# Kernel optimization log

Measured on AMD Instinct MI355X. Metric: run time of the kernel, lower is better.

The kernel has to match this reference:

```python
import jax, jax.numpy as jnp
import numpy as np

N_PTS = 1_000_000
RES = 512
RANK = 48
OUT = 32
INIT_SCALE = 0.1


def _plane_sample(plane, gx, gy):
    """Bilinear grid_sample, align_corners=True, border padding.
    plane: [R, Res, Res] (R=rank); gx, gy: [N] in [-1,1] -> [R, N]."""
    res = plane.shape[-1]
    px = jnp.clip((gx + 1.0) * 0.5 * (res - 1), 0.0, res - 1.0)
    py = jnp.clip((gy + 1.0) * 0.5 * (res - 1), 0.0, res - 1.0)
    x0 = jnp.floor(px).astype(jnp.int32)
    y0 = jnp.floor(py).astype(jnp.int32)
    x1 = jnp.minimum(x0 + 1, res - 1)
    y1 = jnp.minimum(y0 + 1, res - 1)
    wx = px - x0.astype(px.dtype)
    wy = py - y0.astype(py.dtype)
    # gathers: [R, N] each
    v00 = plane[:, y0, x0]
    v01 = plane[:, y0, x1]
    v10 = plane[:, y1, x0]
    v11 = plane[:, y1, x1]
    return (v00 * (1 - wy) * (1 - wx) + v01 * (1 - wy) * wx
            + v10 * wy * (1 - wx) + v11 * wy * wx)


def _line_sample(line, gy):
    """Line is [R, Res] (width dim of size 1 collapses; x coord is 0 -> px=0).
    1-D linear interp along Res with gy in [-1,1] -> [R, N]."""
    res = line.shape[-1]
    py = jnp.clip((gy + 1.0) * 0.5 * (res - 1), 0.0, res - 1.0)
    y0 = jnp.floor(py).astype(jnp.int32)
    y1 = jnp.minimum(y0 + 1, res - 1)
    wy = py - y0.astype(py.dtype)
    return line[:, y0] * (1 - wy) + line[:, y1] * wy


def _geo_forward(coordinates, plane_xy, plane_xz, plane_yz,
                 line_z, line_y, line_x, proj_w, proj_b):
    coords = coordinates * 2.0 - 1.0  # [N, 3] in [-1, 1]
    cx, cy, cz = coords[:, 0], coords[:, 1], coords[:, 2]
    vm = (_plane_sample(plane_xy, cx, cy) * _line_sample(line_z, cz)
          + _plane_sample(plane_xz, cx, cz) * _line_sample(line_y, cy)
          + _plane_sample(plane_yz, cy, cz) * _line_sample(line_x, cx))  # [R, N]
    # projection: [N, R] @ [R, OUT] + b
    return vm.T @ proj_w.T + proj_b


def setup_inputs() -> dict:
    key = jax.random.key(0)
    ks = jax.random.split(key, 9)
    return {
        "coordinates": jax.random.uniform(ks[0], (N_PTS, 3), dtype=jnp.float32),
        "plane_xy": jax.random.normal(ks[1], (RANK, RES, RES), jnp.float32) * INIT_SCALE,
        "plane_xz": jax.random.normal(ks[2], (RANK, RES, RES), jnp.float32) * INIT_SCALE,
        "plane_yz": jax.random.normal(ks[3], (RANK, RES, RES), jnp.float32) * INIT_SCALE,
        "line_z": jax.random.normal(ks[4], (RANK, RES), jnp.float32) * INIT_SCALE,
        "line_y": jax.random.normal(ks[5], (RANK, RES), jnp.float32) * INIT_SCALE,
        "line_x": jax.random.normal(ks[6], (RANK, RES), jnp.float32) * INIT_SCALE,
        "proj_w": jax.random.normal(ks[7], (OUT, RANK), jnp.float32) * INIT_SCALE,
        "proj_b": jnp.zeros((OUT,), jnp.float32),
    }


def reference(coordinates, plane_xy, plane_xz, plane_yz,
              line_z, line_y, line_x, proj_w, proj_b):
    return _geo_forward(coordinates, plane_xy, plane_xz, plane_yz,
                        line_z, line_y, line_x, proj_w, proj_b)
```

## Files before the change

### kernel.cpp

```cpp
#include <hip/hip_runtime.h>
#include <stdint.h>

#define RES      512
#define TEXELS   (RES * RES)
#define NPTS     1000000
#define RANK     48
#define ODIM     32
#define PPB      64
#define VMS      52
#define OSTR     33
#define TT       128
#define TS       25
#define NCELL    4096
#define NB       32
#define SEG      31250
#define ENTR     (NCELL * NB)

typedef unsigned int u32;
typedef float vf4 __attribute__((ext_vector_type(4)));

__device__ __forceinline__ float lobf(u32 u) { return __uint_as_float(u << 16); }
__device__ __forceinline__ float hibf(u32 u) { return __uint_as_float(u & 0xffff0000u); }

__device__ __forceinline__ float ntl(const float* p) {
    return __builtin_nontemporal_load(p);
}
__device__ __forceinline__ vf4 ntl4(const float* p) {
    return __builtin_nontemporal_load((const vf4*)p);
}

__device__ __forceinline__ u32 pkbf(float a, float b) {
    u32 x = __float_as_uint(a), y = __float_as_uint(b);
    u32 xr = (x + 0x7fffu + ((x >> 16) & 1u)) >> 16;
    u32 yr = (y + 0x7fffu + ((y >> 16) & 1u)) & 0xffff0000u;
    return xr | yr;
}

__device__ __forceinline__ u32 sprd4(u32 a) {
    a &= 15u;
    a = (a | (a << 4)) & 0x0C3u;
    a = (a | (a << 2)) & 0x249u;
    return a;
}
__device__ __forceinline__ u32 cellOf(float x, float y, float z) {
    u32 cx = (u32)fminf(fmaxf(x * 16.f, 0.f), 15.f);
    u32 cy = (u32)fminf(fmaxf(y * 16.f, 0.f), 15.f);
    u32 cz = (u32)fminf(fmaxf(z * 16.f, 0.f), 15.f);
    return sprd4(cx) | (sprd4(cy) << 1) | (sprd4(cz) << 2);
}

template <int TEXB>
__global__ __launch_bounds__(256) void transpose_planes(
    const float* __restrict__ p0, const float* __restrict__ p1,
    const float* __restrict__ p2, char* __restrict__ ws)
{
    __shared__ u32 lds[TT * TS + 8];
    int t = threadIdx.x;
    int base = blockIdx.x * TT;
    int plane = blockIdx.y;
    const float* src = (plane == 0) ? p0 : ((plane == 1) ? p1 : p2);
    int xi = t & 31, dg = t >> 5;
#pragma unroll
    for (int j = 0; j < 3; ++j) {
        int d = dg + 8 * j;
        vf4 a = ntl4(src + (size_t)(2 * d) * TEXELS + base + 4 * xi);
        vf4 b = ntl4(src + (size_t)(2 * d + 1) * TEXELS + base + 4 * xi);
        lds[(4 * xi + 0) * TS + d] = pkbf(a.x, b.x);
        lds[(4 * xi + 1) * TS + d] = pkbf(a.y, b.y);
        lds[(4 * xi + 2) * TS + d] = pkbf(a.z, b.z);
        lds[(4 * xi + 3) * TS + d] = pkbf(a.w, b.w);
    }
    __syncthreads();
    char* outp = ws + (size_t)plane * TEXELS * TEXB + (size_t)base * TEXB;
    constexpr int NS = TT * TEXB / (16 * 256);
#pragma unroll
    for (int s = 0; s < NS; ++s) {
        u32 o = (u32)(s * 256 + t) * 16u;
        u32 texel, rem;
        if (TEXB == 128) { texel = o >> 7; rem = o & 127u; }
        else { texel = ((o >> 5) * 43691u) >> 17; rem = o - texel * 96u; }
        u32 dw = texel * TS + (rem >> 2);
        uint4 q = make_uint4(lds[dw], lds[dw + 1], lds[dw + 2], lds[dw + 3]);
        *(uint4*)(outp + o) = q;
    }
}

template <int TEXB>
__global__ __launch_bounds__(256) void transpose_lines(
    const float* __restrict__ lz, const float* __restrict__ ly,
    const float* __restrict__ lx, char* __restrict__ ws)
{
    int id = blockIdx.x * 256 + threadIdx.x;
    int line = id >> 9;
    int pos = id & (RES - 1);
    const float* src = (line == 0) ? lz : ((line == 1) ? ly : lx);
    char* dst = ws + (size_t)3 * TEXELS * TEXB + (size_t)line * RES * TEXB
                   + (size_t)pos * TEXB;
#pragma unroll
    for (int k = 0; k < 6; ++k) {
        uint4 q;
        q.x = pkbf(ntl(&src[(8 * k + 0) * RES + pos]), ntl(&src[(8 * k + 1) * RES + pos]));
        q.y = pkbf(ntl(&src[(8 * k + 2) * RES + pos]), ntl(&src[(8 * k + 3) * RES + pos]));
        q.z = pkbf(ntl(&src[(8 * k + 4) * RES + pos]), ntl(&src[(8 * k + 5) * RES + pos]));
        q.w = pkbf(ntl(&src[(8 * k + 6) * RES + pos]), ntl(&src[(8 * k + 7) * RES + pos]));
        *(uint4*)(dst + 16 * k) = q;
    }
}

__global__ __launch_bounds__(1024) void bin_count(
    const float* __restrict__ coords, u32* __restrict__ T)
{
    __shared__ u32 hist[NCELL];
    int blk = blockIdx.x, t = threadIdx.x;
#pragma unroll
    for (int i = 0; i < NCELL / 1024; ++i) hist[t + 1024 * i] = 0u;
    __syncthreads();
    int lim = (blk + 1) * SEG;
#pragma unroll 1
    for (int it = 0; it < (SEG + 1023) / 1024; ++it) {
        int idx = blk * SEG + it * 1024 + t;
        if (idx < lim) {
            float x = ntl(&coords[3 * idx + 0]);
            float y = ntl(&coords[3 * idx + 1]);
            float z = ntl(&coords[3 * idx + 2]);
            atomicAdd(&hist[cellOf(x, y, z)], 1u);
        }
    }
    __syncthreads();
#pragma unroll
    for (int i = 0; i < NCELL / 1024; ++i) {
        int cell = t + 1024 * i;
        T[(u32)cell * NB + blk] = hist[cell];
    }
}

__global__ __launch_bounds__(1024) void bin_scan(
    const u32* __restrict__ T, u32* __restrict__ C)
{
    __shared__ u32 wt[16];
    int t = threadIdx.x;
    const int PER = ENTR / 1024;
    const u32* tp = T + t * PER;
    u32 tot = 0;
#pragma unroll 16
    for (int i = 0; i < PER; ++i) tot += tp[i];
    int lane = t & 63, w = t >> 6;
    u32 incl = tot;
#pragma unroll
    for (int d = 1; d < 64; d <<= 1) {
        u32 v = __shfl_up(incl, d);
        if (lane >= d) incl += v;
    }
    if (lane == 63) wt[w] = incl;
    __syncthreads();
    u32 run = incl - tot;
#pragma unroll
    for (int i = 0; i < 16; ++i) run += (i < w) ? wt[i] : 0u;
    u32* op = C + t * PER;
#pragma unroll 16
    for (int i = 0; i < PER; ++i) { u32 v = tp[i]; op[i] = run; run += v; }
}

__global__ __launch_bounds__(1024) void bin_scatter(
    const float* __restrict__ coords, const u32* __restrict__ C,
    vf4* __restrict__ rc2)
{
    __shared__ u32 cur[NCELL];
    int blk = blockIdx.x, t = threadIdx.x;
#pragma unroll
    for (int i = 0; i < NCELL / 1024; ++i) {
        int cell = t + 1024 * i;
        cur[cell] = C[(u32)cell * NB + blk];
    }
    __syncthreads();
    int lim = (blk + 1) * SEG;
#pragma unroll 1
    for (int it = 0; it < (SEG + 1023) / 1024; ++it) {
        int idx = blk * SEG + it * 1024 + t;
        if (idx < lim) {
            float x = ntl(&coords[3 * idx + 0]);
            float y = ntl(&coords[3 * idx + 1]);
            float z = ntl(&coords[3 * idx + 2]);
            u32 pos = atomicAdd(&cur[cellOf(x, y, z)], 1u);
            vf4 v; v.x = x; v.y = y; v.z = z; v.w = __uint_as_float((u32)idx);
            __builtin_nontemporal_store(v, rc2 + pos);
        }
    }
}

__device__ __forceinline__ void prep1(float g, int& i0, int& i1, float& w) {
    float p = fminf(fmaxf((g + 1.f) * 0.5f * 511.f, 0.f), 511.f);
    float fp = floorf(p);
    i0 = (int)fp;
    i1 = min(i0 + 1, RES - 1);
    w = p - fp;
}

template <int TEXB, bool SORTED>
__global__ __launch_bounds__(512, 4) void geo_main(
    const void* __restrict__ cin, const char* __restrict__ ws,
    const float* __restrict__ W, const float* __restrict__ Bb,
    float* __restrict__ out)
{
    __shared__ float vm_lds[PPB * VMS];
    __shared__ u32 opt_lds[PPB];

    int tid = threadIdx.x;
    int ptL = tid >> 3;
    int c = tid & 7;

    int bid = blockIdx.x;
    if (SORTED) {
        int nwg = gridDim.x;
        int q = nwg >> 3, r = nwg & 7;
        int xcd = bid & 7, slot = bid >> 3;
        bid = (xcd < r ? xcd * (q + 1) : r * (q + 1) + (xcd - r) * q) + slot;
    }
    int pt = bid * PPB + ptL;

    float gx, gy, gz;
    if (SORTED) {
        vf4 cc = __builtin_nontemporal_load((const vf4*)cin + pt);
        gx = cc.x * 2.f - 1.f;
        gy = cc.y * 2.f - 1.f;
        gz = cc.z * 2.f - 1.f;
        if (c == 0) opt_lds[ptL] = __float_as_uint(cc.w);
    } else {
        const float* coords = (const float*)cin;
        gx = ntl(&coords[3 * pt + 0]) * 2.f - 1.f;
        gy = ntl(&coords[3 * pt + 1]) * 2.f - 1.f;
        gz = ntl(&coords[3 * pt + 2]) * 2.f - 1.f;
        if (c == 0) opt_lds[ptL] = (u32)pt;
    }

    int x0, x1, y0, y1, z0, z1;
    float wx, wy, wz;
    prep1(gx, x0, x1, wx);
    prep1(gy, y0, y1, wy);
    prep1(gz, z0, z1, wz);

    const size_t PW = (size_t)TEXELS * TEXB;
    const size_t LW = (size_t)RES * TEXB;
    const char* pxy = ws;
    const char* pxz = ws + PW;
    const char* pyz = ws + 2 * PW;
    const char* lzb = ws + 3 * PW;
    const char* lyb = lzb + LW;
    const char* lxb = lyb + LW;

    u32 co = 12u * (u32)c;

    u32 q[12][3], le[3][3], lf[3][3];
    {
        u32 offs[12];
        offs[0] = (u32)(y0 * RES + x0) * TEXB + co;
        offs[1] = (u32)(y0 * RES + x1) * TEXB + co;
        offs[2] = (u32)(y1 * RES + x0) * TEXB + co;
        offs[3] = (u32)(y1 * RES + x1) * TEXB + co;
        offs[4] = (u32)(z0 * RES + x0) * TEXB + co;
        offs[5] = (u32)(z0 * RES + x1) * TEXB + co;
        offs[6] = (u32)(z1 * RES + x0) * TEXB + co;
        offs[7] = (u32)(z1 * RES + x1) * TEXB + co;
        offs[8]  = (u32)(z0 * RES + y0) * TEXB + co;
        offs[9]  = (u32)(z0 * RES + y1) * TEXB + co;
        offs[10] = (u32)(z1 * RES + y0) * TEXB + co;
        offs[11] = (u32)(z1 * RES + y1) * TEXB + co;
        const char* bases[3] = { pxy, pxz, pyz };
#pragma unroll
        for (int p = 0; p < 3; ++p) {
#pragma unroll
            for (int k = 0; k < 4; ++k) {
                const u32* s = (const u32*)(bases[p] + offs[4 * p + k]);
                q[4 * p + k][0] = s[0];
                q[4 * p + k][1] = s[1];
                q[4 * p + k][2] = s[2];
            }
        }
        const char* lb[3] = { lzb, lyb, lxb };
        u32 l0[3] = { (u32)z0 * TEXB + co, (u32)y0 * TEXB + co, (u32)x0 * TEXB + co };
        u32 l1[3] = { (u32)z1 * TEXB + co, (u32)y1 * TEXB + co, (u32)x1 * TEXB + co };
#pragma unroll
        for (int p = 0; p < 3; ++p) {
            const u32* s0 = (const u32*)(lb[p] + l0[p]);
            const u32* s1 = (const u32*)(lb[p] + l1[p]);
            le[p][0] = s0[0]; le[p][1] = s0[1]; le[p][2] = s0[2];
            lf[p][0] = s1[0]; lf[p][1] = s1[1]; lf[p][2] = s1[2];
        }
    }

    float pw[3][4];
    pw[0][0] = (1.f - wy) * (1.f - wx); pw[0][1] = (1.f - wy) * wx;
    pw[0][2] = wy * (1.f - wx);         pw[0][3] = wy * wx;
    pw[1][0] = (1.f - wz) * (1.f - wx); pw[1][1] = (1.f - wz) * wx;
    pw[1][2] = wz * (1.f - wx);         pw[1][3] = wz * wx;
    pw[2][0] = (1.f - wz) * (1.f - wy); pw[2][1] = (1.f - wz) * wy;
    pw[2][2] = wz * (1.f - wy);         pw[2][3] = wz * wy;
    float lw[3] = { wz, wy, wx };

    float vm[6] = { 0.f, 0.f, 0.f, 0.f, 0.f, 0.f };
#pragma unroll
    for (int p = 0; p < 3; ++p) {
        float s0 = pw[p][0], s1 = pw[p][1], s2 = pw[p][2], s3 = pw[p][3];
        float il = 1.f - lw[p], wl = lw[p];
#pragma unroll
        for (int d = 0; d < 3; ++d) {
            u32 a = q[4 * p + 0][d], b = q[4 * p + 1][d];
            u32 cc = q[4 * p + 2][d], dd = q[4 * p + 3][d];
            float slo = s0 * lobf(a) + s1 * lobf(b) + s2 * lobf(cc) + s3 * lobf(dd);
            float shi = s0 * hibf(a) + s1 * hibf(b) + s2 * hibf(cc) + s3 * hibf(dd);
            float llo = il * lobf(le[p][d]) + wl * lobf(lf[p][d]);
            float lhi = il * hibf(le[p][d]) + wl * hibf(lf[p][d]);
            vm[2 * d + 0] = fmaf(slo, llo, vm[2 * d + 0]);
            vm[2 * d + 1] = fmaf(shi, lhi, vm[2 * d + 1]);
        }
    }

    float* vr = vm_lds + ptL * VMS + 6 * c;
    *(float2*)(vr + 0) = make_float2(vm[0], vm[1]);
    *(float2*)(vr + 2) = make_float2(vm[2], vm[3]);
    *(float2*)(vr + 4) = make_float2(vm[4], vm[5]);

    __syncthreads();

    int wav = __builtin_amdgcn_readfirstlane(tid >> 6);
    int lane = tid & 63;
    int ob = wav * 4;

    const float* vmrow = vm_lds + lane * VMS;
    float4 bb = *(const float4*)(Bb + ob);
    float a0 = bb.x, a1 = bb.y, a2 = bb.z, a3 = bb.w;
#pragma unroll 4
    for (int k = 0; k < 12; ++k) {
        float4 v = *(const float4*)(vmrow + 4 * k);
        float4 w0 = *(const float4*)(W + (ob + 0) * RANK + 4 * k);
        float4 w1 = *(const float4*)(W + (ob + 1) * RANK + 4 * k);
        float4 w2 = *(const float4*)(W + (ob + 2) * RANK + 4 * k);
        float4 w3 = *(const float4*)(W + (ob + 3) * RANK + 4 * k);
        a0 = fmaf(v.x, w0.x, a0); a0 = fmaf(v.y, w0.y, a0);
        a0 = fmaf(v.z, w0.z, a0); a0 = fmaf(v.w, w0.w, a0);
        a1 = fmaf(v.x, w1.x, a1); a1 = fmaf(v.y, w1.y, a1);
        a1 = fmaf(v.z, w1.z, a1); a1 = fmaf(v.w, w1.w, a1);
        a2 = fmaf(v.x, w2.x, a2); a2 = fmaf(v.y, w2.y, a2);
        a2 = fmaf(v.z, w2.z, a2); a2 = fmaf(v.w, w2.w, a2);
        a3 = fmaf(v.x, w3.x, a3); a3 = fmaf(v.y, w3.y, a3);
        a3 = fmaf(v.z, w3.z, a3); a3 = fmaf(v.w, w3.w, a3);
    }

    __syncthreads();
    {
        vf4 r; r.x = a0; r.y = a1; r.z = a2; r.w = a3;
        *(vf4*)(vm_lds + lane * OSTR + ob) = r;
    }
    __syncthreads();
    {
        int p8 = lane >> 3;
        int c2 = lane & 7;
        int gp = wav * 8 + p8;
        vf4 v = *(const vf4*)(vm_lds + gp * OSTR + 4 * c2);
        size_t orow = (size_t)opt_lds[gp];
        __builtin_nontemporal_store(v, (vf4*)(out + orow * ODIM + 4 * c2));
    }
}

template <int TEXB>
static void launch_unsorted(const float* coords, const float* pxy, const float* pxz,
                            const float* pyz, const float* lz, const float* ly,
                            const float* lx, const float* W, const float* Bb,
                            float* out, char* ws, hipStream_t stream) {
    dim3 gt(TEXELS / TT, 3);
    transpose_planes<TEXB><<<gt, 256, 0, stream>>>(pxy, pxz, pyz, ws);
    transpose_lines<TEXB><<<6, 256, 0, stream>>>(lz, ly, lx, ws);
    geo_main<TEXB, false><<<NPTS / PPB, 512, 0, stream>>>(coords, ws, W, Bb, out);
}

extern "C" void kernel_launch(void* const* d_in, const int* in_sizes, int n_in,
                              void* d_out, int out_size, void* d_ws, size_t ws_size,
                              hipStream_t stream) {
    const float* coords = (const float*)d_in[0];
    const float* pxy = (const float*)d_in[1];
    const float* pxz = (const float*)d_in[2];
    const float* pyz = (const float*)d_in[3];
    const float* lz = (const float*)d_in[4];
    const float* ly = (const float*)d_in[5];
    const float* lx = (const float*)d_in[6];
    const float* W = (const float*)d_in[7];
    const float* Bb = (const float*)d_in[8];
    float* out = (float*)d_out;
    char* ws = (char*)d_ws;

    size_t pool96 = (size_t)3 * TEXELS * 96 + (size_t)3 * RES * 96;
    size_t o_T = (pool96 + 255) & ~(size_t)255;
    size_t o_C = o_T + (size_t)ENTR * 4;
    size_t o_rc2 = o_C + (size_t)ENTR * 4;
    size_t need_sorted = o_rc2 + (size_t)NPTS * 16;
    size_t need128 = (size_t)3 * TEXELS * 128 + (size_t)3 * RES * 128;

    if (ws_size >= need_sorted) {
        u32* T = (u32*)(ws + o_T);
        u32* C = (u32*)(ws + o_C);
        vf4* rc2 = (vf4*)(ws + o_rc2);

        dim3 gt(TEXELS / TT, 3);
        transpose_planes<96><<<gt, 256, 0, stream>>>(pxy, pxz, pyz, ws);
        transpose_lines<96><<<6, 256, 0, stream>>>(lz, ly, lx, ws);
        bin_count<<<NB, 1024, 0, stream>>>(coords, T);
        bin_scan<<<1, 1024, 0, stream>>>(T, C);
        bin_scatter<<<NB, 1024, 0, stream>>>(coords, C, rc2);
        geo_main<96, true><<<NPTS / PPB, 512, 0, stream>>>(rc2, ws, W, Bb, out);
    } else if (ws_size >= need128) {
        launch_unsorted<128>(coords, pxy, pxz, pyz, lz, ly, lx, W, Bb, out, ws, stream);
    } else {
        launch_unsorted<96>(coords, pxy, pxz, pyz, lz, ly, lx, W, Bb, out, ws, stream);
    }
}
```

Before: 493.7 us.

## Fuse transpose and binning prep into one cooperative kernel with grid syncs

```diff
diff --git a/kernel.cpp b/kernel.cpp
--- a/kernel.cpp
+++ b/kernel.cpp
@@ -1,5 +1,8 @@
 #include <hip/hip_runtime.h>
+#include <hip/hip_cooperative_groups.h>
 #include <stdint.h>
+
+namespace cg = cooperative_groups;
 
 #define RES      512
 #define TEXELS   (RES * RES)
@@ -12,9 +15,10 @@
 #define TT       128
 #define TS       25
 #define NCELL    4096
-#define NB       32
-#define SEG      31250
-#define ENTR     (NCELL * NB)
+#define NB       64
+#define SEG      15625
+#define NTILE    6144
+#define NBLK     1024
 
 typedef unsigned int u32;
 typedef float vf4 __attribute__((ext_vector_type(4)));
@@ -49,16 +53,15 @@
     return sprd4(cx) | (sprd4(cy) << 1) | (sprd4(cz) << 2);
 }
 
-template <int TEXB>
-__global__ __launch_bounds__(256) void transpose_planes(
+
+__device__ __forceinline__ void tp_role(int tile, int t,
     const float* __restrict__ p0, const float* __restrict__ p1,
-    const float* __restrict__ p2, char* __restrict__ ws)
-{
-    __shared__ u32 lds[TT * TS + 8];
-    int t = threadIdx.x;
-    int base = blockIdx.x * TT;
-    int plane = blockIdx.y;
+    const float* __restrict__ p2, char* __restrict__ ws, u32* lds)
+{
+    int tno = tile & 2047;
+    int plane = tile >> 11;
     const float* src = (plane == 0) ? p0 : ((plane == 1) ? p1 : p2);
+    int base = tno * TT;
     int xi = t & 31, dg = t >> 5;
 #pragma unroll
     for (int j = 0; j < 3; ++j) {
@@ -71,6 +74,224 @@
         lds[(4 * xi + 3) * TS + d] = pkbf(a.w, b.w);
     }
     __syncthreads();
+    char* outp = ws + (size_t)plane * TEXELS * 96 + (size_t)base * 96;
+#pragma unroll
+    for (int s = 0; s < 3; ++s) {
+        u32 o = (u32)(s * 256 + t) * 16u;
+        u32 texel = ((o >> 5) * 43691u) >> 17;
+        u32 rem = o - texel * 96u;
+        u32 dw = texel * TS + (rem >> 2);
+        uint4 q = make_uint4(lds[dw], lds[dw + 1], lds[dw + 2], lds[dw + 3]);
+        *(uint4*)(outp + o) = q;
+    }
+    __syncthreads();
+}
+
+__device__ __forceinline__ void tp_range(int lo, int hi, int w, int nw, int t,
+    const float* p0, const float* p1, const float* p2, char* ws, u32* lds)
+{
+    for (int tile = lo + w; tile < hi; tile += nw)
+        tp_role(tile, t, p0, p1, p2, ws, lds);
+}
+
+__device__ __forceinline__ void lines_role(int j, int t,
+    const float* __restrict__ lz, const float* __restrict__ ly,
+    const float* __restrict__ lx, char* __restrict__ ws)
+{
+    int id = j * 256 + t;
+    int line = id >> 9;
+    int pos = id & (RES - 1);
+    const float* src = (line == 0) ? lz : ((line == 1) ? ly : lx);
+    char* dst = ws + (size_t)3 * TEXELS * 96 + (size_t)line * RES * 96
+                   + (size_t)pos * 96;
+#pragma unroll
+    for (int k = 0; k < 6; ++k) {
+        uint4 q;
+        q.x = pkbf(ntl(&src[(8 * k + 0) * RES + pos]), ntl(&src[(8 * k + 1) * RES + pos]));
+        q.y = pkbf(ntl(&src[(8 * k + 2) * RES + pos]), ntl(&src[(8 * k + 3) * RES + pos]));
+        q.z = pkbf(ntl(&src[(8 * k + 4) * RES + pos]), ntl(&src[(8 * k + 5) * RES + pos]));
+        q.w = pkbf(ntl(&src[(8 * k + 6) * RES + pos]), ntl(&src[(8 * k + 7) * RES + pos]));
+        *(uint4*)(dst + 16 * k) = q;
+    }
+}
+
+__device__ __forceinline__ void count_role(int blk, int t,
+    const float* __restrict__ coords, u32* __restrict__ T, u32* hist)
+{
+#pragma unroll
+    for (int i = 0; i < NCELL / 256; ++i) hist[t + 256 * i] = 0u;
+    __syncthreads();
+    int lim = (blk + 1) * SEG;
+#pragma unroll 1
+    for (int it = 0; it < (SEG + 255) / 256; ++it) {
+        int idx = blk * SEG + it * 256 + t;
+        if (idx < lim) {
+            float x = ntl(&coords[3 * idx + 0]);
+            float y = ntl(&coords[3 * idx + 1]);
+            float z = ntl(&coords[3 * idx + 2]);
+            atomicAdd(&hist[cellOf(x, y, z)], 1u);
+        }
+    }
+    __syncthreads();
+#pragma unroll
+    for (int i = 0; i < NCELL / 256; ++i) {
+        int cell = t + 256 * i;
+        T[(u32)cell * NB + blk] = hist[cell];
+    }
+}
+
+__device__ __forceinline__ void prefix_role(int bid, int t,
+    u32* __restrict__ T, u32* __restrict__ cellTot)
+{
+    int cell = bid * 256 + t;
+    u32* tp = T + (u32)cell * NB;
+    u32 run = 0;
+#pragma unroll 8
+    for (int b = 0; b < NB; ++b) { u32 v = tp[b]; tp[b] = run; run += v; }
+    cellTot[cell] = run;
+}
+
+__device__ __forceinline__ void base_role(int t,
+    const u32* __restrict__ cellTot, u32* __restrict__ cellBase, u32* wt)
+{
+    u32 loc[16];
+    u32 s = 0;
+#pragma unroll
+    for (int i = 0; i < 16; ++i) { loc[i] = s; s += cellTot[t * 16 + i]; }
+    u32 tot = s;
+    int lane = t & 63, w = t >> 6;
+    u32 incl = tot;
+#pragma unroll
+    for (int d = 1; d < 64; d <<= 1) {
+        u32 v = __shfl_up(incl, d);
+        if (lane >= d) incl += v;
+    }
+    if (lane == 63) wt[w] = incl;
+    __syncthreads();
+    u32 base = incl - tot;
+#pragma unroll
+    for (int i = 0; i < 4; ++i) base += (i < w) ? wt[i] : 0u;
+#pragma unroll
+    for (int i = 0; i < 16; ++i) cellBase[t * 16 + i] = base + loc[i];
+}
+
+__device__ __forceinline__ void scatter_role(int blk, int t,
+    const float* __restrict__ coords, const u32* __restrict__ T,
+    const u32* __restrict__ cellBase, vf4* __restrict__ rc2, u32* cur)
+{
+#pragma unroll
+    for (int i = 0; i < NCELL / 256; ++i) {
+        int cell = t + 256 * i;
+        cur[cell] = cellBase[cell] + T[(u32)cell * NB + blk];
+    }
+    __syncthreads();
+    int lim = (blk + 1) * SEG;
+#pragma unroll 1
+    for (int it = 0; it < (SEG + 255) / 256; ++it) {
+        int idx = blk * SEG + it * 256 + t;
+        if (idx < lim) {
+            float x = ntl(&coords[3 * idx + 0]);
+            float y = ntl(&coords[3 * idx + 1]);
+            float z = ntl(&coords[3 * idx + 2]);
+            u32 pos = atomicAdd(&cur[cellOf(x, y, z)], 1u);
+            vf4 v; v.x = x; v.y = y; v.z = z; v.w = __uint_as_float((u32)idx);
+            __builtin_nontemporal_store(v, rc2 + pos);
+        }
+    }
+}
+
+__global__ void __launch_bounds__(256, 4) prep_all(
+    const float* __restrict__ coords,
+    const float* __restrict__ p0, const float* __restrict__ p1,
+    const float* __restrict__ p2,
+    const float* __restrict__ lz, const float* __restrict__ ly,
+    const float* __restrict__ lx,
+    char* __restrict__ ws, u32* __restrict__ T,
+    u32* __restrict__ cellTot, u32* __restrict__ cellBase,
+    vf4* __restrict__ rc2)
+{
+    __shared__ u32 smem[NCELL + 8];
+    cg::grid_group grid = cg::this_grid();
+    int bid = blockIdx.x, t = threadIdx.x;
+
+    if (bid < NB) count_role(bid, t, coords, T, smem);
+    else          tp_range(0, 2048, bid - NB, NBLK - NB, t, p0, p1, p2, ws, smem);
+    grid.sync();
+
+    if (bid < 16) prefix_role(bid, t, T, cellTot);
+    else          tp_range(2048, 4096, bid - 16, NBLK - 16, t, p0, p1, p2, ws, smem);
+    grid.sync();
+
+    if (bid == 0) base_role(t, cellTot, cellBase, smem);
+    else          tp_range(4096, 5120, bid - 1, NBLK - 1, t, p0, p1, p2, ws, smem);
+    grid.sync();
+
+    if (bid < NB)          scatter_role(bid, t, coords, T, cellBase, rc2, smem);
+    else if (bid < NB + 6) lines_role(bid - NB, t, lz, ly, lx, ws);
+    else                   tp_range(5120, NTILE, bid - NB - 6, NBLK - NB - 6, t,
+                                    p0, p1, p2, ws, smem);
+}
+
+__global__ __launch_bounds__(256) void ser_tp(
+    const float* __restrict__ p0, const float* __restrict__ p1,
+    const float* __restrict__ p2, char* __restrict__ ws)
+{
+    __shared__ u32 smem[NCELL + 8];
+    tp_role(blockIdx.x, threadIdx.x, p0, p1, p2, ws, smem);
+}
+__global__ __launch_bounds__(256) void ser_lines(
+    const float* __restrict__ lz, const float* __restrict__ ly,
+    const float* __restrict__ lx, char* __restrict__ ws)
+{
+    lines_role(blockIdx.x, threadIdx.x, lz, ly, lx, ws);
+}
+__global__ __launch_bounds__(256) void ser_count(
+    const float* __restrict__ coords, u32* __restrict__ T)
+{
+    __shared__ u32 smem[NCELL + 8];
+    count_role(blockIdx.x, threadIdx.x, coords, T, smem);
+}
+__global__ __launch_bounds__(256) void ser_prefix(
+    u32* __restrict__ T, u32* __restrict__ cellTot)
+{
+    prefix_role(blockIdx.x, threadIdx.x, T, cellTot);
+}
+__global__ __launch_bounds__(256) void ser_base(
+    const u32* __restrict__ cellTot, u32* __restrict__ cellBase)
+{
+    __shared__ u32 smem[NCELL + 8];
+    base_role(threadIdx.x, cellTot, cellBase, smem);
+}
+__global__ __launch_bounds__(256) void ser_scatter(
+    const float* __restrict__ coords, const u32* __restrict__ T,
+    const u32* __restrict__ cellBase, vf4* __restrict__ rc2)
+{
+    __shared__ u32 smem[NCELL + 8];
+    scatter_role(blockIdx.x, threadIdx.x, coords, T, cellBase, rc2, smem);
+}
+
+template <int TEXB>
+__global__ __launch_bounds__(256) void transpose_planes(
+    const float* __restrict__ p0, const float* __restrict__ p1,
+    const float* __restrict__ p2, char* __restrict__ ws)
+{
+    __shared__ u32 lds[TT * TS + 8];
+    int t = threadIdx.x;
+    int base = blockIdx.x * TT;
+    int plane = blockIdx.y;
+    const float* src = (plane == 0) ? p0 : ((plane == 1) ? p1 : p2);
+    int xi = t & 31, dg = t >> 5;
+#pragma unroll
+    for (int j = 0; j < 3; ++j) {
+        int d = dg + 8 * j;
+        vf4 a = ntl4(src + (size_t)(2 * d) * TEXELS + base + 4 * xi);
+        vf4 b = ntl4(src + (size_t)(2 * d + 1) * TEXELS + base + 4 * xi);
+        lds[(4 * xi + 0) * TS + d] = pkbf(a.x, b.x);
+        lds[(4 * xi + 1) * TS + d] = pkbf(a.y, b.y);
+        lds[(4 * xi + 2) * TS + d] = pkbf(a.z, b.z);
+        lds[(4 * xi + 3) * TS + d] = pkbf(a.w, b.w);
+    }
+    __syncthreads();
     char* outp = ws + (size_t)plane * TEXELS * TEXB + (size_t)base * TEXB;
     constexpr int NS = TT * TEXB / (16 * 256);
 #pragma unroll
@@ -86,7 +307,7 @@
 }
 
 template <int TEXB>
-__global__ __launch_bounds__(256) void transpose_lines(
+__global__ __launch_bounds__(256) void transpose_lines_t(
     const float* __restrict__ lz, const float* __restrict__ ly,
     const float* __restrict__ lx, char* __restrict__ ws)
 {
@@ -104,87 +325,6 @@
         q.z = pkbf(ntl(&src[(8 * k + 4) * RES + pos]), ntl(&src[(8 * k + 5) * RES + pos]));
         q.w = pkbf(ntl(&src[(8 * k + 6) * RES + pos]), ntl(&src[(8 * k + 7) * RES + pos]));
         *(uint4*)(dst + 16 * k) = q;
-    }
-}
-
-__global__ __launch_bounds__(1024) void bin_count(
-    const float* __restrict__ coords, u32* __restrict__ T)
-{
-    __shared__ u32 hist[NCELL];
-    int blk = blockIdx.x, t = threadIdx.x;
-#pragma unroll
-    for (int i = 0; i < NCELL / 1024; ++i) hist[t + 1024 * i] = 0u;
-    __syncthreads();
-    int lim = (blk + 1) * SEG;
-#pragma unroll 1
-    for (int it = 0; it < (SEG + 1023) / 1024; ++it) {
-        int idx = blk * SEG + it * 1024 + t;
-        if (idx < lim) {
-            float x = ntl(&coords[3 * idx + 0]);
-            float y = ntl(&coords[3 * idx + 1]);
-            float z = ntl(&coords[3 * idx + 2]);
-            atomicAdd(&hist[cellOf(x, y, z)], 1u);
-        }
-    }
-    __syncthreads();
-#pragma unroll
-    for (int i = 0; i < NCELL / 1024; ++i) {
-        int cell = t + 1024 * i;
-        T[(u32)cell * NB + blk] = hist[cell];
-    }
-}
-
-__global__ __launch_bounds__(1024) void bin_scan(
-    const u32* __restrict__ T, u32* __restrict__ C)
-{
-    __shared__ u32 wt[16];
-    int t = threadIdx.x;
-    const int PER = ENTR / 1024;
-    const u32* tp = T + t * PER;
-    u32 tot = 0;
-#pragma unroll 16
-    for (int i = 0; i < PER; ++i) tot += tp[i];
-    int lane = t & 63, w = t >> 6;
-    u32 incl = tot;
-#pragma unroll
-    for (int d = 1; d < 64; d <<= 1) {
-        u32 v = __shfl_up(incl, d);
-        if (lane >= d) incl += v;
-    }
-    if (lane == 63) wt[w] = incl;
-    __syncthreads();
-    u32 run = incl - tot;
-#pragma unroll
-    for (int i = 0; i < 16; ++i) run += (i < w) ? wt[i] : 0u;
-    u32* op = C + t * PER;
-#pragma unroll 16
-    for (int i = 0; i < PER; ++i) { u32 v = tp[i]; op[i] = run; run += v; }
-}
-
-__global__ __launch_bounds__(1024) void bin_scatter(
-    const float* __restrict__ coords, const u32* __restrict__ C,
-    vf4* __restrict__ rc2)
-{
-    __shared__ u32 cur[NCELL];
-    int blk = blockIdx.x, t = threadIdx.x;
-#pragma unroll
-    for (int i = 0; i < NCELL / 1024; ++i) {
-        int cell = t + 1024 * i;
-        cur[cell] = C[(u32)cell * NB + blk];
-    }
-    __syncthreads();
-    int lim = (blk + 1) * SEG;
-#pragma unroll 1
-    for (int it = 0; it < (SEG + 1023) / 1024; ++it) {
-        int idx = blk * SEG + it * 1024 + t;
-        if (idx < lim) {
-            float x = ntl(&coords[3 * idx + 0]);
-            float y = ntl(&coords[3 * idx + 1]);
-            float z = ntl(&coords[3 * idx + 2]);
-            u32 pos = atomicAdd(&cur[cellOf(x, y, z)], 1u);
-            vf4 v; v.x = x; v.y = y; v.z = z; v.w = __uint_as_float((u32)idx);
-            __builtin_nontemporal_store(v, rc2 + pos);
-        }
     }
 }
 
@@ -369,7 +509,7 @@
                             float* out, char* ws, hipStream_t stream) {
     dim3 gt(TEXELS / TT, 3);
     transpose_planes<TEXB><<<gt, 256, 0, stream>>>(pxy, pxz, pyz, ws);
-    transpose_lines<TEXB><<<6, 256, 0, stream>>>(lz, ly, lx, ws);
+    transpose_lines_t<TEXB><<<6, 256, 0, stream>>>(lz, ly, lx, ws);
     geo_main<TEXB, false><<<NPTS / PPB, 512, 0, stream>>>(coords, ws, W, Bb, out);
 }
 
@@ -390,22 +530,32 @@
 
     size_t pool96 = (size_t)3 * TEXELS * 96 + (size_t)3 * RES * 96;
     size_t o_T = (pool96 + 255) & ~(size_t)255;
-    size_t o_C = o_T + (size_t)ENTR * 4;
-    size_t o_rc2 = o_C + (size_t)ENTR * 4;
+    size_t o_ct = o_T + (size_t)NCELL * NB * 4;
+    size_t o_cb = o_ct + (size_t)NCELL * 4;
+    size_t o_rc2 = o_cb + (size_t)NCELL * 4;
     size_t need_sorted = o_rc2 + (size_t)NPTS * 16;
     size_t need128 = (size_t)3 * TEXELS * 128 + (size_t)3 * RES * 128;
 
     if (ws_size >= need_sorted) {
         u32* T = (u32*)(ws + o_T);
-        u32* C = (u32*)(ws + o_C);
+        u32* cellTot = (u32*)(ws + o_ct);
+        u32* cellBase = (u32*)(ws + o_cb);
         vf4* rc2 = (vf4*)(ws + o_rc2);
 
-        dim3 gt(TEXELS / TT, 3);
-        transpose_planes<96><<<gt, 256, 0, stream>>>(pxy, pxz, pyz, ws);
-        transpose_lines<96><<<6, 256, 0, stream>>>(lz, ly, lx, ws);
-        bin_count<<<NB, 1024, 0, stream>>>(coords, T);
-        bin_scan<<<1, 1024, 0, stream>>>(T, C);
-        bin_scatter<<<NB, 1024, 0, stream>>>(coords, C, rc2);
+        void* args[] = { (void*)&coords, (void*)&pxy, (void*)&pxz, (void*)&pyz,
+                         (void*)&lz, (void*)&ly, (void*)&lx,
+                         (void*)&ws, (void*)&T, (void*)&cellTot,
+                         (void*)&cellBase, (void*)&rc2 };
+        hipError_t err = hipLaunchCooperativeKernel(
+            (const void*)prep_all, dim3(NBLK), dim3(256), args, 0, stream);
+        if (err != hipSuccess) {
+            ser_tp<<<NTILE, 256, 0, stream>>>(pxy, pxz, pyz, ws);
+            ser_lines<<<6, 256, 0, stream>>>(lz, ly, lx, ws);
+            ser_count<<<NB, 256, 0, stream>>>(coords, T);
+            ser_prefix<<<16, 256, 0, stream>>>(T, cellTot);
+            ser_base<<<1, 256, 0, stream>>>(cellTot, cellBase);
+            ser_scatter<<<NB, 256, 0, stream>>>(coords, T, cellBase, rc2);
+        }
         geo_main<96, true><<<NPTS / PPB, 512, 0, stream>>>(rc2, ws, W, Bb, out);
     } else if (ws_size >= need128) {
         launch_unsorted<128>(coords, pxy, pxz, pyz, lz, ly, lx, W, Bb, out, ws, stream);
```

Result: slower. 837.8 us (+69.7%).
